# Kernel optimization log

Hardware: AMD Instinct MI355X
Metric: run time of the kernel (lower is better)

The kernel has to match this reference:

```python
import jax, jax.numpy as jnp
import numpy as np

B, IN_F, OUT_F = 1024, 512, 512


def setup_inputs() -> dict:
    key = jax.random.key(0)
    k1, k2 = jax.random.split(key)
    x = jax.random.uniform(k1, (B, IN_F), dtype=jnp.float32)
    weight = jax.random.uniform(k2, (IN_F, OUT_F), dtype=jnp.float32)
    return {"x": x, "weight": weight}


def reference(x, weight):
    # Max-min fuzzy composition (tropical semiring 'matmul'):
    # out[b, o] = max_i min(x[b, i], W[i, o])
    # x: [B, IN], weight: [IN, OUT] -> out: [B, OUT]
    return jnp.max(jnp.minimum(x[:, :, None], weight[None, :, :]), axis=1)
```

## Files before the change

kernel.cpp:

```cpp
#include <hip/hip_runtime.h>


typedef unsigned int u32;
typedef u32 u32x2 __attribute__((ext_vector_type(2)));
typedef u32 u32x4 __attribute__((ext_vector_type(4)));
typedef float f4 __attribute__((ext_vector_type(4)));
typedef float f2 __attribute__((ext_vector_type(2)));
typedef __fp16 h2 __attribute__((ext_vector_type(2)));

#define XB 8192
#define WB 16384
#define BUFB (XB + WB)

static __device__ __forceinline__ u32 pkcvt(float a, float b) {
  return __builtin_bit_cast(u32, __builtin_amdgcn_cvt_pkrtz(a, b));
}
static __device__ __forceinline__ u32 pkmax(u32 a, u32 b) {
  u32 d; asm("v_pk_max_u16 %0, %1, %2" : "=v"(d) : "v"(a), "v"(b)); return d;
}
static __device__ __forceinline__ u32 pkmin_bl(u32 x, u32 w) {
  u32 d;
  asm("v_pk_min_u16 %0, %1, %2 op_sel:[0,0] op_sel_hi:[0,1]"
      : "=v"(d) : "v"(x), "v"(w));
  return d;
}
static __device__ __forceinline__ u32 pkmin_bh(u32 x, u32 w) {
  u32 d;
  asm("v_pk_min_u16 %0, %1, %2 op_sel:[1,0] op_sel_hi:[1,1]"
      : "=v"(d) : "v"(x), "v"(w));
  return d;
}
static __device__ __forceinline__ u32 halfswap_max(u32 v) {
  u32 a = v, b = v;
  asm("v_permlane32_swap_b32 %0, %1" : "+v"(a), "+v"(b));
  return pkmax(a, b);
}

__global__ __launch_bounds__(1024, 4) void maxmin_v6(const float* __restrict__ X,
                                                     const float* __restrict__ W,
                                                     float* __restrict__ Out) {
  __shared__ __align__(16) char smem[65536];

  const int tid  = threadIdx.x;
  const int wv   = tid >> 6;
  const int lane = tid & 63;
  const int sh   = lane >> 5;
  const int l5   = lane & 31;
  const int ty   = l5 >> 3;
  const int tx   = l5 & 7;
  const int b0   = blockIdx.x * 32;
  const int o0   = blockIdx.y * 64;

  const int xr  = tid >> 5;
  const int xkq = tid & 31;
  const float* xg = X + (b0 + xr) * 512 + xkq * 4;
  const int xw0 = (2 * xkq) * 128 + 4 * (xr ^ ((2 * xkq) & 28));

  const int wkk = tid >> 4;
  const int wc4 = tid & 15;
  const float* wg = W + wkk * 512 + o0 + wc4 * 4;
  const int ww0 = XB + wkk * 128 + wc4 * 8;

  const int kpb = 4 * wv + 2 * sh;
  const int wro = XB + 16 * tx;

  u32 acc[8][4] = {};

  auto stage = [&](char* buf, f4 xv, f4 wa, f4 wb) {
    *(u32*)(buf + xw0)       = pkcvt(xv.x, xv.y);
    *(u32*)(buf + xw0 + 128) = pkcvt(xv.z, xv.w);
    u32x2 wpa = {pkcvt(wa.x, wa.y), pkcvt(wa.z, wa.w)};
    *(u32x2*)(buf + ww0) = wpa;
    u32x2 wpb = {pkcvt(wb.x, wb.y), pkcvt(wb.z, wb.w)};
    *(u32x2*)(buf + ww0 + 64 * 128) = wpb;
  };

  {
    f4 xv = *(const f4*)xg;
    f4 wa = *(const f4*)wg;
    f4 wb = *(const f4*)(wg + 64 * 512);
    stage(smem, xv, wa, wb);
  }
  __syncthreads();

  for (int c = 0; c < 4; ++c) {
    f4 nx = {}, na = {}, nb = {};
    if (c < 3) {
      nx = *(const f4*)(xg + (c + 1) * 128);
      na = *(const f4*)(wg + (c + 1) * 128 * 512);
      nb = *(const f4*)(wg + (c + 1) * 128 * 512 + 64 * 512);
    }
    const char* buf = smem + (c & 1) * BUFB;
#pragma unroll
    for (int q = 0; q < 2; ++q) {
      const int kp = kpb + q;
      const int m  = kp & 28;
      u32x4 x0 = *(const u32x4*)(buf + kp * 128 + 4 * ((8 * ty) ^ m));
      u32x4 x1 = *(const u32x4*)(buf + kp * 128 + 4 * ((8 * ty + 4) ^ m));
      u32x4 wl = *(const u32x4*)(buf + wro + (2 * kp) * 128);
      u32x4 wh = *(const u32x4*)(buf + wro + (2 * kp) * 128 + 128);
#pragma unroll
      for (int j = 0; j < 4; ++j)
#pragma unroll
        for (int cc = 0; cc < 4; ++cc) {
          acc[j][cc]     = pkmax(acc[j][cc],     pkmin_bl(x0[j], wl[cc]));
          acc[j][cc]     = pkmax(acc[j][cc],     pkmin_bh(x0[j], wh[cc]));
          acc[4 + j][cc] = pkmax(acc[4 + j][cc], pkmin_bl(x1[j], wl[cc]));
          acc[4 + j][cc] = pkmax(acc[4 + j][cc], pkmin_bh(x1[j], wh[cc]));
        }
    }
    if (c < 3) stage(smem + ((c + 1) & 1) * BUFB, nx, na, nb);
    __syncthreads();
  }

#pragma unroll
  for (int j = 0; j < 8; ++j)
#pragma unroll
    for (int cc = 0; cc < 4; ++cc) acc[j][cc] = halfswap_max(acc[j][cc]);

  if (sh == 0) {
#pragma unroll
    for (int j = 0; j < 8; ++j) {
      u32x4 v = {acc[j][0], acc[j][1], acc[j][2], acc[j][3]};
      *(u32x4*)(smem + wv * 4096 + (8 * ty + j) * 128 + tx * 16) = v;
    }
  }
  __syncthreads();

  const int row = tid >> 5;
  const int cp  = tid & 31;
  const int cb  = row * 128 + cp * 4;
  u32 m = *(const u32*)(smem + cb);
#pragma unroll
  for (int g = 1; g < 16; ++g) m = pkmax(m, *(const u32*)(smem + g * 4096 + cb));
  h2 hm = __builtin_bit_cast(h2, m);
  f2 o = {(float)hm.x, (float)hm.y};
  *(f2*)(Out + (b0 + row) * 512 + o0 + cp * 2) = o;
}

extern "C" void kernel_launch(void* const* d_in, const int* in_sizes, int n_in,
                              void* d_out, int out_size, void* d_ws, size_t ws_size,
                              hipStream_t stream) {
  const float* x = (const float*)d_in[0];
  const float* w = (const float*)d_in[1];
  float* out = (float*)d_out;
  (void)in_sizes; (void)n_in; (void)out_size; (void)d_ws; (void)ws_size;
  dim3 grid(1024 / 32, 512 / 64);
  maxmin_v6<<<grid, 1024, 0, stream>>>(x, w, out);
}
```

Before: 67.87 us.

## Shrink block to 16 rows with 512 threads and padded LDS strides

Moves from 1024-thread blocks covering 32 batch rows to 512-thread blocks covering 16 rows, which doubles the grid. Replaces the XOR-swizzled shared layout with padded row strides (80/144 bytes) and loads weights as four contiguous float4 per thread. The k-split reduction changes from two half-waves to four quarter-waves, adding a shuffle-xor step before the permlane swap. Smaller blocks and less LDS per block aim to improve occupancy and scheduling, at the cost of twice the total weight traffic from global memory and a longer intra-wave reduction.

```diff
diff --git a/kernel.cpp b/kernel.cpp
--- a/kernel.cpp
+++ b/kernel.cpp
@@ -2,15 +2,16 @@
 
 
 typedef unsigned int u32;
-typedef u32 u32x2 __attribute__((ext_vector_type(2)));
 typedef u32 u32x4 __attribute__((ext_vector_type(4)));
 typedef float f4 __attribute__((ext_vector_type(4)));
 typedef float f2 __attribute__((ext_vector_type(2)));
 typedef __fp16 h2 __attribute__((ext_vector_type(2)));
 
-#define XB 8192
-#define WB 16384
-#define BUFB (XB + WB)
+#define XSTRIDE 80
+#define WSTRIDE 144
+#define XB2 (64 * XSTRIDE)
+#define WB2 (128 * WSTRIDE)
+#define BUFB2 (XB2 + WB2)
 
 static __device__ __forceinline__ u32 pkcvt(float a, float b) {
   return __builtin_bit_cast(u32, __builtin_amdgcn_cvt_pkrtz(a, b));
@@ -36,69 +37,67 @@
   return pkmax(a, b);
 }
 
-__global__ __launch_bounds__(1024, 4) void maxmin_v6(const float* __restrict__ X,
-                                                     const float* __restrict__ W,
-                                                     float* __restrict__ Out) {
-  __shared__ __align__(16) char smem[65536];
+__global__ __launch_bounds__(512, 4) void maxmin_v7(const float* __restrict__ X,
+                                                    const float* __restrict__ W,
+                                                    float* __restrict__ Out) {
+  __shared__ __align__(16) char smem[2 * BUFB2];
 
   const int tid  = threadIdx.x;
   const int wv   = tid >> 6;
   const int lane = tid & 63;
-  const int sh   = lane >> 5;
-  const int l5   = lane & 31;
-  const int ty   = l5 >> 3;
-  const int tx   = l5 & 7;
-  const int b0   = blockIdx.x * 32;
+  const int qw   = lane >> 4;
+  const int ty   = (lane >> 3) & 1;
+  const int tx   = lane & 7;
+  const int b0   = blockIdx.x * 16;
   const int o0   = blockIdx.y * 64;
 
-  const int xr  = tid >> 5;
-  const int xkq = tid & 31;
-  const float* xg = X + (b0 + xr) * 512 + xkq * 4;
-  const int xw0 = (2 * xkq) * 128 + 4 * (xr ^ ((2 * xkq) & 28));
+  const int xr  = tid & 15;
+  const int xq4 = tid >> 4;
+  const float* xg = X + (b0 + xr) * 512 + 4 * xq4;
+  const int xw0 = (2 * xq4) * XSTRIDE + 4 * xr;
 
-  const int wkk = tid >> 4;
-  const int wc4 = tid & 15;
-  const float* wg = W + wkk * 512 + o0 + wc4 * 4;
-  const int ww0 = XB + wkk * 128 + wc4 * 8;
+  const int wkk = tid >> 2;
+  const int wc  = tid & 3;
+  const float* wg = W + wkk * 512 + o0 + 16 * wc;
+  const int ww0 = XB2 + wkk * WSTRIDE + 32 * wc;
 
-  const int kpb = 4 * wv + 2 * sh;
-  const int wro = XB + 16 * tx;
+  const int kpb = 8 * wv + 2 * qw;
 
   u32 acc[8][4] = {};
 
-  auto stage = [&](char* buf, f4 xv, f4 wa, f4 wb) {
-    *(u32*)(buf + xw0)       = pkcvt(xv.x, xv.y);
-    *(u32*)(buf + xw0 + 128) = pkcvt(xv.z, xv.w);
-    u32x2 wpa = {pkcvt(wa.x, wa.y), pkcvt(wa.z, wa.w)};
-    *(u32x2*)(buf + ww0) = wpa;
-    u32x2 wpb = {pkcvt(wb.x, wb.y), pkcvt(wb.z, wb.w)};
-    *(u32x2*)(buf + ww0 + 64 * 128) = wpb;
+  auto stage = [&](char* buf, f4 xv, f4 w0, f4 w1, f4 w2, f4 w3) {
+    *(u32*)(buf + xw0)           = pkcvt(xv.x, xv.y);
+    *(u32*)(buf + xw0 + XSTRIDE) = pkcvt(xv.z, xv.w);
+    u32x4 pa = {pkcvt(w0.x, w0.y), pkcvt(w0.z, w0.w),
+                pkcvt(w1.x, w1.y), pkcvt(w1.z, w1.w)};
+    u32x4 pb = {pkcvt(w2.x, w2.y), pkcvt(w2.z, w2.w),
+                pkcvt(w3.x, w3.y), pkcvt(w3.z, w3.w)};
+    *(u32x4*)(buf + ww0)      = pa;
+    *(u32x4*)(buf + ww0 + 16) = pb;
   };
 
   {
     f4 xv = *(const f4*)xg;
-    f4 wa = *(const f4*)wg;
-    f4 wb = *(const f4*)(wg + 64 * 512);
-    stage(smem, xv, wa, wb);
+    const f4* wp = (const f4*)wg;
+    stage(smem, xv, wp[0], wp[1], wp[2], wp[3]);
   }
   __syncthreads();
 
   for (int c = 0; c < 4; ++c) {
-    f4 nx = {}, na = {}, nb = {};
+    f4 nx = {}, n0 = {}, n1 = {}, n2 = {}, n3 = {};
     if (c < 3) {
       nx = *(const f4*)(xg + (c + 1) * 128);
-      na = *(const f4*)(wg + (c + 1) * 128 * 512);
-      nb = *(const f4*)(wg + (c + 1) * 128 * 512 + 64 * 512);
+      const f4* wp = (const f4*)(wg + (c + 1) * 128 * 512);
+      n0 = wp[0]; n1 = wp[1]; n2 = wp[2]; n3 = wp[3];
     }
-    const char* buf = smem + (c & 1) * BUFB;
+    const char* buf = smem + (c & 1) * BUFB2;
 #pragma unroll
     for (int q = 0; q < 2; ++q) {
       const int kp = kpb + q;
-      const int m  = kp & 28;
-      u32x4 x0 = *(const u32x4*)(buf + kp * 128 + 4 * ((8 * ty) ^ m));
-      u32x4 x1 = *(const u32x4*)(buf + kp * 128 + 4 * ((8 * ty + 4) ^ m));
-      u32x4 wl = *(const u32x4*)(buf + wro + (2 * kp) * 128);
-      u32x4 wh = *(const u32x4*)(buf + wro + (2 * kp) * 128 + 128);
+      u32x4 x0 = *(const u32x4*)(buf + kp * XSTRIDE + 32 * ty);
+      u32x4 x1 = *(const u32x4*)(buf + kp * XSTRIDE + 32 * ty + 16);
+      u32x4 wl = *(const u32x4*)(buf + XB2 + (2 * kp) * WSTRIDE + 16 * tx);
+      u32x4 wh = *(const u32x4*)(buf + XB2 + (2 * kp) * WSTRIDE + WSTRIDE + 16 * tx);
 #pragma unroll
       for (int j = 0; j < 4; ++j)
 #pragma unroll
@@ -109,20 +108,24 @@
           acc[4 + j][cc] = pkmax(acc[4 + j][cc], pkmin_bh(x1[j], wh[cc]));
         }
     }
-    if (c < 3) stage(smem + ((c + 1) & 1) * BUFB, nx, na, nb);
+    if (c < 3) stage(smem + ((c + 1) & 1) * BUFB2, nx, n0, n1, n2, n3);
     __syncthreads();
   }
 
 #pragma unroll
   for (int j = 0; j < 8; ++j)
 #pragma unroll
-    for (int cc = 0; cc < 4; ++cc) acc[j][cc] = halfswap_max(acc[j][cc]);
+    for (int cc = 0; cc < 4; ++cc) {
+      u32 v = acc[j][cc];
+      v = pkmax(v, (u32)__shfl_xor((int)v, 16, 64));
+      acc[j][cc] = halfswap_max(v);
+    }
 
-  if (sh == 0) {
+  if (qw == 0) {
 #pragma unroll
     for (int j = 0; j < 8; ++j) {
       u32x4 v = {acc[j][0], acc[j][1], acc[j][2], acc[j][3]};
-      *(u32x4*)(smem + wv * 4096 + (8 * ty + j) * 128 + tx * 16) = v;
+      *(u32x4*)(smem + wv * 2048 + (8 * ty + j) * 128 + tx * 16) = v;
     }
   }
   __syncthreads();
@@ -132,7 +135,7 @@
   const int cb  = row * 128 + cp * 4;
   u32 m = *(const u32*)(smem + cb);
 #pragma unroll
-  for (int g = 1; g < 16; ++g) m = pkmax(m, *(const u32*)(smem + g * 4096 + cb));
+  for (int g = 1; g < 8; ++g) m = pkmax(m, *(const u32*)(smem + g * 2048 + cb));
   h2 hm = __builtin_bit_cast(h2, m);
   f2 o = {(float)hm.x, (float)hm.y};
   *(f2*)(Out + (b0 + row) * 512 + o0 + cp * 2) = o;
@@ -145,6 +148,6 @@
   const float* w = (const float*)d_in[1];
   float* out = (float*)d_out;
   (void)in_sizes; (void)n_in; (void)out_size; (void)d_ws; (void)ws_size;
-  dim3 grid(1024 / 32, 512 / 64);
-  maxmin_v6<<<grid, 1024, 0, stream>>>(x, w, out);
+  dim3 grid(1024 / 16, 512 / 64);
+  maxmin_v7<<<grid, 512, 0, stream>>>(x, w, out);
 }
```

Result: slower. 69.35 us (+2.2%).

## Stage all K chunks into shared memory up front and drop per-chunk barriers

Applied to the files above, without the earlier changes.

Replaces the double-buffered loop over four K chunks with a single prologue. The prologue issues all global loads for X and W at once, converts them to fp16 and writes them into four separate LDS buffers. The compute loop then runs across all chunks with no barriers in between, and one barrier is added before the reduction reuses shared memory. This aims to expose more memory-level parallelism and remove three block-wide syncs. In exchange, LDS per block grows to about 96KB and register pressure rises from holding twelve float4 loads at once.

```diff
diff --git a/kernel.cpp b/kernel.cpp
--- a/kernel.cpp
+++ b/kernel.cpp
@@ -36,10 +36,10 @@
   return pkmax(a, b);
 }
 
-__global__ __launch_bounds__(1024, 4) void maxmin_v6(const float* __restrict__ X,
+__global__ __launch_bounds__(1024, 4) void maxmin_v8(const float* __restrict__ X,
                                                      const float* __restrict__ W,
                                                      float* __restrict__ Out) {
-  __shared__ __align__(16) char smem[65536];
+  __shared__ __align__(16) char smem[4 * BUFB];
 
   const int tid  = threadIdx.x;
   const int wv   = tid >> 6;
@@ -66,31 +66,30 @@
 
   u32 acc[8][4] = {};
 
-  auto stage = [&](char* buf, f4 xv, f4 wa, f4 wb) {
-    *(u32*)(buf + xw0)       = pkcvt(xv.x, xv.y);
-    *(u32*)(buf + xw0 + 128) = pkcvt(xv.z, xv.w);
-    u32x2 wpa = {pkcvt(wa.x, wa.y), pkcvt(wa.z, wa.w)};
-    *(u32x2*)(buf + ww0) = wpa;
-    u32x2 wpb = {pkcvt(wb.x, wb.y), pkcvt(wb.z, wb.w)};
-    *(u32x2*)(buf + ww0 + 64 * 128) = wpb;
-  };
-
   {
-    f4 xv = *(const f4*)xg;
-    f4 wa = *(const f4*)wg;
-    f4 wb = *(const f4*)(wg + 64 * 512);
-    stage(smem, xv, wa, wb);
+    f4 xv[4], wa[4], wb[4];
+#pragma unroll
+    for (int c = 0; c < 4; ++c) {
+      xv[c] = *(const f4*)(xg + c * 128);
+      wa[c] = *(const f4*)(wg + c * 128 * 512);
+      wb[c] = *(const f4*)(wg + c * 128 * 512 + 64 * 512);
+    }
+#pragma unroll
+    for (int c = 0; c < 4; ++c) {
+      char* buf = smem + c * BUFB;
+      *(u32*)(buf + xw0)       = pkcvt(xv[c].x, xv[c].y);
+      *(u32*)(buf + xw0 + 128) = pkcvt(xv[c].z, xv[c].w);
+      u32x2 wpa = {pkcvt(wa[c].x, wa[c].y), pkcvt(wa[c].z, wa[c].w)};
+      *(u32x2*)(buf + ww0) = wpa;
+      u32x2 wpb = {pkcvt(wb[c].x, wb[c].y), pkcvt(wb[c].z, wb[c].w)};
+      *(u32x2*)(buf + ww0 + 64 * 128) = wpb;
+    }
   }
   __syncthreads();
 
+#pragma unroll
   for (int c = 0; c < 4; ++c) {
-    f4 nx = {}, na = {}, nb = {};
-    if (c < 3) {
-      nx = *(const f4*)(xg + (c + 1) * 128);
-      na = *(const f4*)(wg + (c + 1) * 128 * 512);
-      nb = *(const f4*)(wg + (c + 1) * 128 * 512 + 64 * 512);
-    }
-    const char* buf = smem + (c & 1) * BUFB;
+    const char* buf = smem + c * BUFB;
 #pragma unroll
     for (int q = 0; q < 2; ++q) {
       const int kp = kpb + q;
@@ -109,14 +108,14 @@
           acc[4 + j][cc] = pkmax(acc[4 + j][cc], pkmin_bh(x1[j], wh[cc]));
         }
     }
-    if (c < 3) stage(smem + ((c + 1) & 1) * BUFB, nx, na, nb);
-    __syncthreads();
   }
 
 #pragma unroll
   for (int j = 0; j < 8; ++j)
 #pragma unroll
     for (int cc = 0; cc < 4; ++cc) acc[j][cc] = halfswap_max(acc[j][cc]);
+
+  __syncthreads();
 
   if (sh == 0) {
 #pragma unroll
@@ -146,5 +145,5 @@
   float* out = (float*)d_out;
   (void)in_sizes; (void)n_in; (void)out_size; (void)d_ws; (void)ws_size;
   dim3 grid(1024 / 32, 512 / 64);
-  maxmin_v6<<<grid, 1024, 0, stream>>>(x, w, out);
+  maxmin_v8<<<grid, 1024, 0, stream>>>(x, w, out);
 }
```

Measured after the change: 67.40 us. Within noise of the previous version (-0.7%).
